# Kernel optimization log

Hardware: AMD Instinct MI355X
Metric: run time of the kernel (lower is better)

## Reference

```python
import jax, jax.numpy as jnp
import numpy as np

D_EMB = 1024
N_HEADS = 16


def setup_inputs() -> dict:
    key = jax.random.key(0)
    k_x, k_wq, k_bq, k_wp, k_bp = jax.random.split(key, 5)
    B, N, D = 8, 1024, D_EMB
    x = jax.random.normal(k_x, (B, N, D), dtype=jnp.float32)
    s = 1.0 / np.sqrt(D)
    w_qkv = jax.random.normal(k_wq, (D, 3 * D), dtype=jnp.float32) * s
    b_qkv = jax.random.normal(k_bq, (3 * D,), dtype=jnp.float32) * 0.01
    w_proj = jax.random.normal(k_wp, (D, D), dtype=jnp.float32) * s
    b_proj = jax.random.normal(k_bp, (D,), dtype=jnp.float32) * 0.01
    return {"x": x, "w_qkv": w_qkv, "b_qkv": b_qkv, "w_proj": w_proj, "b_proj": b_proj}


def reference(x, w_qkv, b_qkv, w_proj, b_proj):
    B, N, D = x.shape
    H = N_HEADS
    d = D // H
    qkv = x @ w_qkv + b_qkv                      # [B, N, 3D]
    # einops '(h d qkv)': qkv index is the innermost factor of the last dim
    qkv = qkv.reshape(B, N, H, d, 3)
    q = qkv[..., 0]                              # [B, N, H, d]
    k = qkv[..., 1]
    v = qkv[..., 2]
    score = jnp.einsum('bqhd,bkhd->bhqk', q, k)  # [B, H, N, N]
    # module scales AFTER softmax, by sqrt(d_emb) (not sqrt(d_head))
    att = jax.nn.softmax(score, axis=-1) / jnp.sqrt(jnp.float32(D))
    out = jnp.einsum('bhqk,bkhd->bqhd', att, v).reshape(B, N, D)
    return out @ w_proj + b_proj
```

## Files before the change

### kernel.cpp

```cpp
#include <hip/hip_runtime.h>
#include <hip/hip_bf16.h>
#include <stdint.h>

typedef __hip_bfloat16 bf16;
typedef __attribute__((ext_vector_type(8))) short short8;
typedef __attribute__((ext_vector_type(4))) float f32x4;
typedef __attribute__((ext_vector_type(16))) float f32x16;

#define MFMA16(a, b, c) __builtin_amdgcn_mfma_f32_16x16x32_bf16(a, b, c, 0, 0, 0)
#define MFMA32(a, b, c) __builtin_amdgcn_mfma_f32_32x32x16_bf16(a, b, c, 0, 0, 0)

#define BATCH 8
#define SEQ   1024
#define DEMB  1024
#define NH    16
#define DH    64
#define MTOT  (BATCH * SEQ)
#define LOG2E 1.44269504088896340736f

__device__ __forceinline__ float rdf(const void* p, size_t idx, int isf) {
  if (isf) return ((const float*)p)[idx];
  return __bfloat162float(((const bf16*)p)[idx]);
}

__device__ __forceinline__ unsigned int pk2(float a, float b) {
  unsigned short ua = __bfloat16_as_ushort(__float2bfloat16(a));
  unsigned short ub = __bfloat16_as_ushort(__float2bfloat16(b));
  return (unsigned int)ua | ((unsigned int)ub << 16);
}

union U4S8 { uint4 u; short8 s; };

__device__ __forceinline__ void gload16(const bf16* g, bf16* l) {
  __builtin_amdgcn_global_load_lds(
      (const __attribute__((address_space(1))) void*)g,
      (__attribute__((address_space(3))) void*)l, 16, 0, 0);
}

__global__ void detect_dtype(const unsigned int* __restrict__ xw, int* __restrict__ flag) {
  int lane = threadIdx.x;
  float v = __uint_as_float(xw[lane]);
  bool isf32 = (fabsf(v) < 1e20f);
  unsigned long long m = __ballot(isf32);
  if (lane == 0) flag[0] = (__popcll(m) >= 32) ? 1 : 0;
}

__global__ __launch_bounds__(256) void convert_x(
    const void* __restrict__ xin, bf16* __restrict__ xc, const int* __restrict__ flag) {
  const int isf = flag[0];
  size_t i = ((size_t)blockIdx.x * 256 + threadIdx.x) * 8;
  if (isf) {
    const float* xf = (const float*)xin;
    float4 a = *(const float4*)&xf[i];
    float4 b = *(const float4*)&xf[i + 4];
    bf16 o[8];
    o[0] = __float2bfloat16(a.x); o[1] = __float2bfloat16(a.y);
    o[2] = __float2bfloat16(a.z); o[3] = __float2bfloat16(a.w);
    o[4] = __float2bfloat16(b.x); o[5] = __float2bfloat16(b.y);
    o[6] = __float2bfloat16(b.z); o[7] = __float2bfloat16(b.w);
    *(int4*)&xc[i] = *(const int4*)&o[0];
  } else {
    *(int4*)&xc[i] = *(const int4*)&((const bf16*)xin)[i];
  }
}

__global__ __launch_bounds__(256) void permute_wqkv(
    const void* __restrict__ w, const void* __restrict__ b,
    bf16* __restrict__ wt, float* __restrict__ bqp, const int* __restrict__ flag) {
  __shared__ __attribute__((aligned(16))) bf16 ls[192][66];
  const int isf = flag[0];
  const int t = threadIdx.x;
  const int k0 = blockIdx.x * 64;
  const int h = blockIdx.y;
#pragma unroll
  for (int i = 0; i < 48; ++i) {
    int e = t + i * 256;
    int k = e / 192, c = e % 192;
    ls[c][k] = __float2bfloat16(rdf(w, (size_t)(k0 + k) * 3072 + h * 192 + c, isf));
  }
  if (blockIdx.x == 0 && t < 192) {
    int dd = t / 3, j = t % 3;
    bqp[j * 1024 + h * 64 + dd] = rdf(b, h * 192 + t, isf);
  }
  __syncthreads();
#pragma unroll
  for (int i = 0; i < 48; ++i) {
    int e = t + i * 256;
    int c = e / 64, k = e & 63;
    int dd = c / 3, j = c % 3;
    wt[(size_t)(j * 1024 + h * 64 + dd) * 1024 + k0 + k] = ls[c][k];
  }
}

__global__ __launch_bounds__(256) void transpose_wp(
    const void* __restrict__ w, bf16* __restrict__ wt, const int* __restrict__ flag) {
  __shared__ __attribute__((aligned(16))) bf16 ls[64][66];
  const int isf = flag[0];
  const int t = threadIdx.x;
  const int r0 = blockIdx.y * 64;
  const int c0 = blockIdx.x * 64;
#pragma unroll
  for (int i = 0; i < 16; ++i) {
    int e = t + i * 256;
    int r = e >> 6, c = e & 63;
    ls[c][r] = __float2bfloat16(rdf(w, (size_t)(r0 + r) * 1024 + c0 + c, isf));
  }
  __syncthreads();
#pragma unroll
  for (int i = 0; i < 16; ++i) {
    int e = t + i * 256;
    int c = e >> 6, r = e & 63;
    wt[(size_t)(c0 + c) * 1024 + r0 + r] = ls[c][r];
  }
}

__device__ __forceinline__ void gemm128x256_core(
    const bf16* __restrict__ A, const bf16* __restrict__ Bt,
    int m0, int n0, bf16* lds, f32x4 acc[4][4]) {
  const int t = threadIdx.x;
  const int lane = t & 63, w = t >> 6;
  const int l15 = lane & 15, quad = lane >> 4;
  const int wm = w >> 2, wn = w & 3;
  const int sr = lane >> 2;
  const int scs = (((lane & 3) ^ ((lane >> 3) & 3))) * 8;
  const bf16* gA = A + (size_t)(m0 + w * 16 + sr) * 1024 + scs;
  const bf16* gB = Bt + (size_t)(n0 + w * 16 + sr) * 1024 + scs;

#pragma unroll
  for (int tt = 0; tt < 3; ++tt) {
    bf16* sb = lds + tt * 12288;
    gload16(gA + tt * 32, sb + w * 512);
    gload16(gB + tt * 32, sb + 4096 + w * 512);
    gload16(gB + tt * 32 + 131072, sb + 8192 + w * 512);
  }
  asm volatile("s_waitcnt vmcnt(6)" ::: "memory");
  __builtin_amdgcn_s_barrier();

  const int swz8 = ((quad ^ (l15 >> 1)) & 3) * 8;
  const bf16* paBase = lds + (wm * 64 + l15) * 32 + swz8;
  const bf16* pbBase = lds + 4096 + (wn * 64 + l15) * 32 + swz8;

#pragma unroll 4
  for (int tau = 0; tau < 32; ++tau) {
    const int slot = tau & 3;
    const int pf = (tau + 3) & 3;
    const int kpf = ((tau + 3) & 31) * 32;
    const bf16* pa = paBase + slot * 12288;
    const bf16* pb = pbBase + slot * 12288;
    bf16* sb = lds + pf * 12288;
    short8 afr[4], bfr[4];
#pragma unroll
    for (int i = 0; i < 4; ++i) afr[i] = *(const short8*)(pa + i * 512);
#pragma unroll
    for (int j = 0; j < 4; ++j) bfr[j] = *(const short8*)(pb + j * 512);
    gload16(gA + kpf, sb + w * 512);
    gload16(gB + kpf, sb + 4096 + w * 512);
    gload16(gB + kpf + 131072, sb + 8192 + w * 512);
    asm volatile("" ::: "memory");
    __builtin_amdgcn_s_barrier();
    asm volatile("s_waitcnt lgkmcnt(0)" ::: "memory");
    __builtin_amdgcn_s_setprio(1);
#pragma unroll
    for (int i = 0; i < 4; ++i)
#pragma unroll
      for (int j = 0; j < 4; ++j)
        acc[i][j] = MFMA16(afr[i], bfr[j], acc[i][j]);
    __builtin_amdgcn_s_setprio(0);
    asm volatile("s_waitcnt vmcnt(6)" ::: "memory");
    asm volatile("" ::: "memory");
    __builtin_amdgcn_s_barrier();
  }
  asm volatile("s_waitcnt vmcnt(0)" ::: "memory");
}

__global__ __launch_bounds__(512, 2) void gemm_qkv(
    const bf16* __restrict__ A, const bf16* __restrict__ Bt,
    const float* __restrict__ bias,
    bf16* __restrict__ qb, bf16* __restrict__ kb, bf16* __restrict__ vb) {
  extern __shared__ bf16 smem[];
  const int t = threadIdx.x;
  const int lane = t & 63;
  const int l15 = lane & 15, quad = lane >> 4;
  const int w = t >> 6, wm = w >> 2, wn = w & 3;
  const int bid = blockIdx.x;
  const int swz = (bid & 7) * 96 + (bid >> 3);
  const int m0 = (swz / 12) * 128;
  const int n0 = (swz % 12) * 256;

  f32x4 acc[4][4];
  const f32x4 zero = {0.f, 0.f, 0.f, 0.f};
#pragma unroll
  for (int i = 0; i < 4; ++i)
#pragma unroll
    for (int j = 0; j < 4; ++j) acc[i][j] = zero;

  gemm128x256_core(A, Bt, m0, n0, smem, acc);

  const int jj = n0 >> 10;
  const int hh = ((n0 + wn * 64) & 1023) >> 6;
  const float qscale = (jj == 0) ? LOG2E : 1.0f;
#pragma unroll
  for (int fi = 0; fi < 4; ++fi) {
    int m = m0 + wm * 64 + fi * 16 + quad * 4;
    int bb = m >> 10, nidx = m & 1023;
    size_t bhq = (size_t)(bb * NH + hh);
#pragma unroll
    for (int fj = 0; fj < 4; ++fj) {
      int dd = fj * 16 + l15;
      float bv = bias[n0 + wn * 64 + dd];
      if (jj == 2) {
        unsigned int lo = pk2(acc[fi][fj][0] + bv, acc[fi][fj][1] + bv);
        unsigned int hi = pk2(acc[fi][fj][2] + bv, acc[fi][fj][3] + bv);
        *(uint2*)&vb[(bhq * 64 + dd) * 1024 + nidx] = make_uint2(lo, hi);
      } else {
        bf16* dst = (jj == 0) ? qb : kb;
#pragma unroll
        for (int r = 0; r < 4; ++r)
          dst[(bhq * 1024 + (size_t)(nidx + r)) * 64 + dd] =
              __float2bfloat16((acc[fi][fj][r] + bv) * qscale);
      }
    }
  }
}

__global__ __launch_bounds__(256, 4) void attn(
    const bf16* __restrict__ qb, const bf16* __restrict__ kb,
    const bf16* __restrict__ vb, bf16* __restrict__ ob) {
  const int t = threadIdx.x, lane = t & 63, w = t >> 6;
  const int q5 = lane & 31, half = lane >> 5;
  const int bh = blockIdx.y;
  const int bat = bh >> 4, h = bh & 15;
  const int q0 = blockIdx.x * 128;
  const int qrow = q0 + w * 32 + q5;

  __shared__ __attribute__((aligned(16))) bf16 lsK[64][72];
  __shared__ __attribute__((aligned(16))) bf16 lsV[64][72];

  const bf16* qp = qb + (size_t)bh * (1024 * 64);
  const bf16* kp = kb + (size_t)bh * (1024 * 64);
  const bf16* vp = vb + (size_t)bh * (64 * 1024);

  short8 bq[4];
#pragma unroll
  for (int kk = 0; kk < 4; ++kk)
    bq[kk] = *(const short8*)&qp[(size_t)qrow * 64 + kk * 16 + half * 8];

  float l_run = 0.f;
  f32x16 po[2];
#pragma unroll
  for (int r = 0; r < 16; ++r) { po[0][r] = 0.f; po[1][r] = 0.f; }

  const int sr = t >> 3;
  const int sc = (t & 7) * 8;

  int4 g0 = *(const int4*)&kp[(size_t)sr * 64 + sc];
  int4 g1 = *(const int4*)&kp[(size_t)(32 + sr) * 64 + sc];
  int4 g2 = *(const int4*)&vp[(size_t)sr * 1024 + sc];
  int4 g3 = *(const int4*)&vp[(size_t)(32 + sr) * 1024 + sc];

  for (int kt = 0; kt < 1024; kt += 64) {
    __syncthreads();
    *(int4*)&lsK[sr][sc] = g0;
    *(int4*)&lsK[32 + sr][sc] = g1;
    *(int4*)&lsV[sr][sc] = g2;
    *(int4*)&lsV[32 + sr][sc] = g3;
    __syncthreads();

    const int ktn = kt + 64;
    if (ktn < 1024) {
      g0 = *(const int4*)&kp[(size_t)(ktn + sr) * 64 + sc];
      g1 = *(const int4*)&kp[(size_t)(ktn + 32 + sr) * 64 + sc];
      g2 = *(const int4*)&vp[(size_t)sr * 1024 + ktn + sc];
      g3 = *(const int4*)&vp[(size_t)(32 + sr) * 1024 + ktn + sc];
    }

    f32x16 st[2];
#pragma unroll
    for (int r = 0; r < 16; ++r) { st[0][r] = 0.f; st[1][r] = 0.f; }
#pragma unroll
    for (int kk = 0; kk < 4; ++kk) {
#pragma unroll
      for (int tj = 0; tj < 2; ++tj) {
        short8 ak = *(const short8*)&lsK[tj * 32 + q5][kk * 16 + half * 8];
        st[tj] = MFMA32(ak, bq[kk], st[tj]);
      }
    }

    float lsum = 0.f;
#pragma unroll
    for (int tj = 0; tj < 2; ++tj)
#pragma unroll
      for (int r = 0; r < 16; ++r) {
        float p = exp2f(st[tj][r]);
        st[tj][r] = p;
        lsum += p;
      }
    l_run += lsum;

#pragma unroll
    for (int kk2 = 0; kk2 < 4; ++kk2) {
      const int nbA = 2 * kk2, nbB = 2 * kk2 + 1;
      unsigned int a0 = pk2(st[nbA >> 2][4 * (nbA & 3) + 0], st[nbA >> 2][4 * (nbA & 3) + 1]);
      unsigned int a1 = pk2(st[nbA >> 2][4 * (nbA & 3) + 2], st[nbA >> 2][4 * (nbA & 3) + 3]);
      unsigned int b0 = pk2(st[nbB >> 2][4 * (nbB & 3) + 0], st[nbB >> 2][4 * (nbB & 3) + 1]);
      unsigned int b1 = pk2(st[nbB >> 2][4 * (nbB & 3) + 2], st[nbB >> 2][4 * (nbB & 3) + 3]);
      unsigned int s0 = half ? a0 : b0;
      unsigned int s1 = half ? a1 : b1;
      unsigned int r0 = (unsigned int)__shfl_xor((int)s0, 32);
      unsigned int r1 = (unsigned int)__shfl_xor((int)s1, 32);
      U4S8 fr;
      fr.u.x = half ? r0 : a0;
      fr.u.y = half ? r1 : a1;
      fr.u.z = half ? b0 : r0;
      fr.u.w = half ? b1 : r1;
#pragma unroll
      for (int ti = 0; ti < 2; ++ti) {
        short8 av = *(const short8*)&lsV[ti * 32 + q5][kk2 * 16 + half * 8];
        po[ti] = MFMA32(av, fr.s, po[ti]);
      }
    }
  }

  l_run += __shfl_xor(l_run, 32);
  float inv = 1.0f / (l_run * 32.0f);
  bf16* op = ob + ((size_t)(bat * 1024 + qrow)) * 1024 + h * 64;
#pragma unroll
  for (int ti = 0; ti < 2; ++ti)
#pragma unroll
    for (int g = 0; g < 4; ++g) {
      unsigned int lo = pk2(po[ti][4 * g + 0] * inv, po[ti][4 * g + 1] * inv);
      unsigned int hi = pk2(po[ti][4 * g + 2] * inv, po[ti][4 * g + 3] * inv);
      uint2 u = make_uint2(lo, hi);
      *(uint2*)&op[ti * 32 + g * 8 + half * 4] = u;
    }
}

__global__ __launch_bounds__(512, 2) void gemm_proj(
    const bf16* __restrict__ A, const bf16* __restrict__ Bt,
    const void* __restrict__ bias, float* __restrict__ out,
    const int* __restrict__ flag) {
  extern __shared__ bf16 smem[];
  const int t = threadIdx.x;
  const int lane = t & 63;
  const int l15 = lane & 15, quad = lane >> 4;
  const int w = t >> 6, wm = w >> 2, wn = w & 3;
  const int bid = blockIdx.x;
  const int swz = (bid & 7) * 32 + (bid >> 3);
  const int m0 = (swz >> 2) * 128;
  const int n0 = (swz & 3) * 256;

  f32x4 acc[4][4];
  const f32x4 zero = {0.f, 0.f, 0.f, 0.f};
#pragma unroll
  for (int i = 0; i < 4; ++i)
#pragma unroll
    for (int j = 0; j < 4; ++j) acc[i][j] = zero;

  gemm128x256_core(A, Bt, m0, n0, smem, acc);

  const int isf = flag[0];
#pragma unroll
  for (int fj = 0; fj < 4; ++fj) {
    int c = n0 + wn * 64 + fj * 16 + l15;
    float bv = rdf(bias, c, isf);
#pragma unroll
    for (int fi = 0; fi < 4; ++fi) {
      int m = m0 + wm * 64 + fi * 16 + quad * 4;
#pragma unroll
      for (int r = 0; r < 4; ++r)
        out[(size_t)(m + r) * 1024 + c] = acc[fi][fj][r] + bv;
    }
  }
}

extern "C" void kernel_launch(void* const* d_in, const int* in_sizes, int n_in,
                              void* d_out, int out_size, void* d_ws, size_t ws_size,
                              hipStream_t stream) {
  const void* x      = d_in[0];
  const void* w_qkv  = d_in[1];
  const void* b_qkv  = d_in[2];
  const void* w_proj = d_in[3];
  const void* b_proj = d_in[4];
  float* out = (float*)d_out;

  char* ws = (char*)d_ws;
  bf16*  wt_qkv = (bf16*)(ws);
  float* bqp    = (float*)(ws + 6291456);
  bf16*  wtp    = (bf16*)(ws + 6303744);
  bf16*  xc     = (bf16*)(ws + 8400896);
  bf16*  q_buf  = (bf16*)(ws + 25178112);
  bf16*  k_buf  = (bf16*)(ws + 41955328);
  bf16*  v_buf  = (bf16*)(ws + 58732544);
  int*   flag   = (int*)(ws + 75509760);
  bf16*  att    = xc;

  static bool lds_attr_done = false;
  if (!lds_attr_done) {
    (void)hipFuncSetAttribute(reinterpret_cast<const void*>(gemm_qkv),
                              hipFuncAttributeMaxDynamicSharedMemorySize, 98304);
    (void)hipFuncSetAttribute(reinterpret_cast<const void*>(gemm_proj),
                              hipFuncAttributeMaxDynamicSharedMemorySize, 98304);
    lds_attr_done = true;
  }

  detect_dtype<<<1, 64, 0, stream>>>((const unsigned int*)x, flag);
  convert_x<<<4096, 256, 0, stream>>>(x, xc, flag);
  permute_wqkv<<<dim3(16, 16), 256, 0, stream>>>(w_qkv, b_qkv, wt_qkv, bqp, flag);
  transpose_wp<<<dim3(16, 16), 256, 0, stream>>>(w_proj, wtp, flag);
  gemm_qkv<<<dim3(768), 512, 98304, stream>>>(xc, wt_qkv, bqp, q_buf, k_buf, v_buf);
  attn<<<dim3(8, 128), 256, 0, stream>>>(q_buf, k_buf, v_buf, att);
  gemm_proj<<<dim3(256), 512, 98304, stream>>>(att, wtp, b_proj, out, flag);
}
```

Before: 277.5 us.

## Double-buffer LDS fragments in GEMM core and enlarge QKV tile to 256x256

Reworks the shared GEMM main loop so each iteration reads the next k-slice's LDS fragments into a second register buffer while issuing MFMAs on the current one. This removes the lgkmcnt wait and one barrier per step. The QKV GEMM now uses 256x256 tiles (MF=8), with half as many blocks and 128 KB of LDS. The goal is more reuse per block and more MFMA work per barrier, at the cost of more registers and LDS, which may lower occupancy below the two blocks per CU the launch bounds request.

```diff
diff --git a/kernel.cpp b/kernel.cpp
--- a/kernel.cpp
+++ b/kernel.cpp
@@ -114,9 +114,12 @@
   }
 }
 
-__device__ __forceinline__ void gemm128x256_core(
+template <int MF>
+__device__ __forceinline__ void gemm_core_pipe(
     const bf16* __restrict__ A, const bf16* __restrict__ Bt,
-    int m0, int n0, bf16* lds, f32x4 acc[4][4]) {
+    int m0, int n0, bf16* lds, f32x4 acc[MF][4]) {
+  constexpr int ASLOT = MF * 1024;
+  constexpr int SLOT  = ASLOT + 8192;
   const int t = threadIdx.x;
   const int lane = t & 63, w = t >> 6;
   const int l15 = lane & 15, quad = lane >> 4;
@@ -128,47 +131,55 @@
 
 #pragma unroll
   for (int tt = 0; tt < 3; ++tt) {
-    bf16* sb = lds + tt * 12288;
+    bf16* sb = lds + tt * SLOT;
     gload16(gA + tt * 32, sb + w * 512);
-    gload16(gB + tt * 32, sb + 4096 + w * 512);
-    gload16(gB + tt * 32 + 131072, sb + 8192 + w * 512);
-  }
-  asm volatile("s_waitcnt vmcnt(6)" ::: "memory");
+    if (MF == 8) gload16(gA + tt * 32 + 131072, sb + 4096 + w * 512);
+    gload16(gB + tt * 32, sb + ASLOT + w * 512);
+    gload16(gB + tt * 32 + 131072, sb + ASLOT + 4096 + w * 512);
+  }
+  if (MF == 8) { asm volatile("s_waitcnt vmcnt(4)" ::: "memory"); }
+  else         { asm volatile("s_waitcnt vmcnt(3)" ::: "memory"); }
   __builtin_amdgcn_s_barrier();
+  asm volatile("" ::: "memory");
 
   const int swz8 = ((quad ^ (l15 >> 1)) & 3) * 8;
-  const bf16* paBase = lds + (wm * 64 + l15) * 32 + swz8;
-  const bf16* pbBase = lds + 4096 + (wn * 64 + l15) * 32 + swz8;
+  const int paOff = (wm * (MF * 16) + l15) * 32 + swz8;
+  const int pbOff = ASLOT + (wn * 64 + l15) * 32 + swz8;
+
+  short8 fa[2][MF], fb[2][4];
+#pragma unroll
+  for (int i = 0; i < MF; ++i) fa[0][i] = *(const short8*)(lds + paOff + i * 512);
+#pragma unroll
+  for (int j = 0; j < 4; ++j)  fb[0][j] = *(const short8*)(lds + pbOff + j * 512);
 
 #pragma unroll 4
   for (int tau = 0; tau < 32; ++tau) {
-    const int slot = tau & 3;
-    const int pf = (tau + 3) & 3;
+    const int cu = tau & 1, nx = cu ^ 1;
+    const int s_nxt = (tau + 1) & 3;
+    const int s_pf = (tau + 3) & 3;
     const int kpf = ((tau + 3) & 31) * 32;
-    const bf16* pa = paBase + slot * 12288;
-    const bf16* pb = pbBase + slot * 12288;
-    bf16* sb = lds + pf * 12288;
-    short8 afr[4], bfr[4];
-#pragma unroll
-    for (int i = 0; i < 4; ++i) afr[i] = *(const short8*)(pa + i * 512);
-#pragma unroll
-    for (int j = 0; j < 4; ++j) bfr[j] = *(const short8*)(pb + j * 512);
+    bf16* sb = lds + s_pf * SLOT;
     gload16(gA + kpf, sb + w * 512);
-    gload16(gB + kpf, sb + 4096 + w * 512);
-    gload16(gB + kpf + 131072, sb + 8192 + w * 512);
+    if (MF == 8) gload16(gA + kpf + 131072, sb + 4096 + w * 512);
+    gload16(gB + kpf, sb + ASLOT + w * 512);
+    gload16(gB + kpf + 131072, sb + ASLOT + 4096 + w * 512);
     asm volatile("" ::: "memory");
+    __builtin_amdgcn_s_setprio(1);
+    const bf16* ls = lds + s_nxt * SLOT;
+#pragma unroll
+    for (int i = 0; i < MF; ++i) fa[nx][i] = *(const short8*)(ls + paOff + i * 512);
+#pragma unroll
+    for (int j = 0; j < 4; ++j)  fb[nx][j] = *(const short8*)(ls + pbOff + j * 512);
+#pragma unroll
+    for (int i = 0; i < MF; ++i)
+#pragma unroll
+      for (int j = 0; j < 4; ++j)
+        acc[i][j] = MFMA16(fa[cu][i], fb[cu][j], acc[i][j]);
+    __builtin_amdgcn_s_setprio(0);
+    if (MF == 8) { asm volatile("s_waitcnt vmcnt(4)" ::: "memory"); }
+    else         { asm volatile("s_waitcnt vmcnt(3)" ::: "memory"); }
     __builtin_amdgcn_s_barrier();
-    asm volatile("s_waitcnt lgkmcnt(0)" ::: "memory");
-    __builtin_amdgcn_s_setprio(1);
-#pragma unroll
-    for (int i = 0; i < 4; ++i)
-#pragma unroll
-      for (int j = 0; j < 4; ++j)
-        acc[i][j] = MFMA16(afr[i], bfr[j], acc[i][j]);
-    __builtin_amdgcn_s_setprio(0);
-    asm volatile("s_waitcnt vmcnt(6)" ::: "memory");
     asm volatile("" ::: "memory");
-    __builtin_amdgcn_s_barrier();
   }
   asm volatile("s_waitcnt vmcnt(0)" ::: "memory");
 }
@@ -183,25 +194,25 @@
   const int l15 = lane & 15, quad = lane >> 4;
   const int w = t >> 6, wm = w >> 2, wn = w & 3;
   const int bid = blockIdx.x;
-  const int swz = (bid & 7) * 96 + (bid >> 3);
-  const int m0 = (swz / 12) * 128;
+  const int swz = (bid & 7) * 48 + (bid >> 3);
+  const int m0 = (swz / 12) * 256;
   const int n0 = (swz % 12) * 256;
 
-  f32x4 acc[4][4];
+  f32x4 acc[8][4];
   const f32x4 zero = {0.f, 0.f, 0.f, 0.f};
 #pragma unroll
-  for (int i = 0; i < 4; ++i)
+  for (int i = 0; i < 8; ++i)
 #pragma unroll
     for (int j = 0; j < 4; ++j) acc[i][j] = zero;
 
-  gemm128x256_core(A, Bt, m0, n0, smem, acc);
+  gemm_core_pipe<8>(A, Bt, m0, n0, smem, acc);
 
   const int jj = n0 >> 10;
   const int hh = ((n0 + wn * 64) & 1023) >> 6;
   const float qscale = (jj == 0) ? LOG2E : 1.0f;
 #pragma unroll
-  for (int fi = 0; fi < 4; ++fi) {
-    int m = m0 + wm * 64 + fi * 16 + quad * 4;
+  for (int fi = 0; fi < 8; ++fi) {
+    int m = m0 + wm * 128 + fi * 16 + quad * 4;
     int bb = m >> 10, nidx = m & 1023;
     size_t bhq = (size_t)(bb * NH + hh);
 #pragma unroll
@@ -356,7 +367,7 @@
 #pragma unroll
     for (int j = 0; j < 4; ++j) acc[i][j] = zero;
 
-  gemm128x256_core(A, Bt, m0, n0, smem, acc);
+  gemm_core_pipe<4>(A, Bt, m0, n0, smem, acc);
 
   const int isf = flag[0];
 #pragma unroll
@@ -397,7 +408,7 @@
   static bool lds_attr_done = false;
   if (!lds_attr_done) {
     (void)hipFuncSetAttribute(reinterpret_cast<const void*>(gemm_qkv),
-                              hipFuncAttributeMaxDynamicSharedMemorySize, 98304);
+                              hipFuncAttributeMaxDynamicSharedMemorySize, 131072);
     (void)hipFuncSetAttribute(reinterpret_cast<const void*>(gemm_proj),
                               hipFuncAttributeMaxDynamicSharedMemorySize, 98304);
     lds_attr_done = true;
@@ -407,7 +418,7 @@
   convert_x<<<4096, 256, 0, stream>>>(x, xc, flag);
   permute_wqkv<<<dim3(16, 16), 256, 0, stream>>>(w_qkv, b_qkv, wt_qkv, bqp, flag);
   transpose_wp<<<dim3(16, 16), 256, 0, stream>>>(w_proj, wtp, flag);
-  gemm_qkv<<<dim3(768), 512, 98304, stream>>>(xc, wt_qkv, bqp, q_buf, k_buf, v_buf);
+  gemm_qkv<<<dim3(384), 512, 131072, stream>>>(xc, wt_qkv, bqp, q_buf, k_buf, v_buf);
   attn<<<dim3(8, 128), 256, 0, stream>>>(q_buf, k_buf, v_buf, att);
   gemm_proj<<<dim3(256), 512, 98304, stream>>>(att, wtp, b_proj, out, flag);
 }
```

Result: no change. 275.0 us (-0.9%).
